# Kernel tuning notes

Hardware: AMD Instinct MI355X
Metric: run time of the kernel (lower is better)

## Reference

```python
import jax, jax.numpy as jnp
import numpy as np

B, L, D = 2, 2048, 1024
H, DK, DV = 16, 64, 64
LN_EPS = 1e-6


def setup_inputs() -> dict:
    key = jax.random.key(0)
    ks = jax.random.split(key, 8)
    s = 0.02
    return {
        "q": jax.random.normal(ks[0], (B, L, D), jnp.float32),
        "k": jax.random.normal(ks[1], (B, L, D), jnp.float32),
        "v": jax.random.normal(ks[2], (B, L, D), jnp.float32),
        "mask": jnp.ones((B, L, L), jnp.int32),
        "w_q": jax.random.normal(ks[3], (D, H * DK), jnp.float32) * s,
        "w_k": jax.random.normal(ks[4], (D, H * DK), jnp.float32) * s,
        "w_v": jax.random.normal(ks[5], (D, H * DV), jnp.float32) * s,
        "w_fc": jax.random.normal(ks[6], (H * DV, D), jnp.float32) * s,
        "ln_g": jnp.ones((D,), jnp.float32),
        "ln_b": jnp.zeros((D,), jnp.float32),
    }


def reference(q, k, v, mask, w_q, w_k, w_v, w_fc, ln_g, ln_b):
    b, lq, d = q.shape
    residual = q
    # QKV projections, split heads: (B, H, L, dk)
    qh = (q @ w_q).reshape(b, lq, H, DK).transpose(0, 2, 1, 3)
    kh = (k @ w_k).reshape(b, -1, H, DK).transpose(0, 2, 1, 3)
    vh = (v @ w_v).reshape(b, -1, H, DV).transpose(0, 2, 1, 3)
    scale = DK ** 0.5
    attn = jnp.einsum("bhqd,bhkd->bhqk", qh / scale, kh)
    attn = jnp.where(mask[:, None, :, :] == 0, -1e9, attn)
    attn = jax.nn.softmax(attn, axis=-1)  # dropout is identity in eval
    out = jnp.einsum("bhqk,bhkd->bhqd", attn, vh)
    out = out.transpose(0, 2, 1, 3).reshape(b, lq, H * DV)
    out = out @ w_fc + residual
    # LayerNorm (eps=1e-6)
    mu = out.mean(-1, keepdims=True)
    var = out.var(-1, keepdims=True)
    out = (out - mu) * jax.lax.rsqrt(var + LN_EPS) * ln_g + ln_b
    return out, attn
```

## Files before the change

kernel.cpp:

```cpp
#include <hip/hip_runtime.h>
#include <math.h>

static constexpr int Bc = 2;
static constexpr int Lc = 2048;
static constexpr int Dc = 1024;
static constexpr int Hc = 16;
static constexpr int DKc = 64;

typedef unsigned short u16;
typedef __attribute__((ext_vector_type(8))) short s16x8;
typedef __attribute__((ext_vector_type(4))) float f32x4;
typedef __attribute__((ext_vector_type(4))) unsigned short u16x4;

#define MFMA(a, b, c) __builtin_amdgcn_mfma_f32_16x16x32_bf16((a), (b), (c), 0, 0, 0)

__device__ __forceinline__ u16 f2bf(float f) {
    unsigned int u = __float_as_uint(f);
    u += 0x7fff + ((u >> 16) & 1);
    return (u16)(u >> 16);
}

__device__ __forceinline__ int swz(int row, int u) {
    return (row << 6) + ((u ^ (row & 7)) << 3);
}

__device__ __forceinline__ float blockReduce(float val, float* red) {
    __syncthreads();
    #pragma unroll
    for (int o = 32; o > 0; o >>= 1) val += __shfl_down(val, o, 64);
    const int lane = threadIdx.x & 63;
    const int wid = threadIdx.x >> 6;
    if (lane == 0) red[wid] = val;
    __syncthreads();
    if (threadIdx.x == 0) {
        float r = red[0];
        #pragma unroll
        for (int i = 1; i < 4; ++i) r += red[i];
        red[0] = r;
    }
    __syncthreads();
    return red[0];
}

__global__ __launch_bounds__(256) void k_wprep(const float* __restrict__ W,
                                               u16* __restrict__ Wt) {
    __shared__ float T[64][65];
    const int t = threadIdx.x;
    const int n0 = blockIdx.x * 64, k0 = blockIdx.y * 64;
    #pragma unroll
    for (int i = 0; i < 16; ++i) {
        int flat = t + i * 256;
        int r = flat >> 6, c = flat & 63;
        T[r][c] = W[(size_t)(k0 + r) * Dc + n0 + c];
    }
    __syncthreads();
    #pragma unroll
    for (int i = 0; i < 16; ++i) {
        int flat = t + i * 256;
        int r = flat >> 6, c = flat & 63;
        Wt[(size_t)(n0 + r) * Dc + k0 + c] = f2bf(T[c][r]);
    }
}

template<int MODE>
__global__ __launch_bounds__(256) void k_gemm(const void* __restrict__ Ap,
                                              const u16* __restrict__ Bt,
                                              const float* __restrict__ RES,
                                              void* __restrict__ Yp) {
    __shared__ u16 As[64 * 64];
    __shared__ u16 Bs[128 * 64];
    const int t = threadIdx.x;
    const int lane = t & 63, wid = t >> 6;
    const int wm = wid >> 1, wn = wid & 1;
    const int row0 = blockIdx.x * 64, col0 = blockIdx.y * 128;
    f32x4 acc[2][4] = {};
    for (int kt = 0; kt < Dc; kt += 64) {
        if constexpr (MODE == 0) {
            const float* A = (const float*)Ap;
            #pragma unroll
            for (int i = 0; i < 2; ++i) {
                int flat = t + i * 256;
                int r = flat >> 3, u = flat & 7;
                const float4* src = (const float4*)(A + (size_t)(row0 + r) * Dc + kt + u * 8);
                float4 x = src[0], y = src[1];
                union { s16x8 v; u16 q[8]; } pk;
                pk.q[0] = f2bf(x.x); pk.q[1] = f2bf(x.y); pk.q[2] = f2bf(x.z); pk.q[3] = f2bf(x.w);
                pk.q[4] = f2bf(y.x); pk.q[5] = f2bf(y.y); pk.q[6] = f2bf(y.z); pk.q[7] = f2bf(y.w);
                *(s16x8*)&As[swz(r, u)] = pk.v;
            }
        } else {
            const u16* A = (const u16*)Ap;
            #pragma unroll
            for (int i = 0; i < 2; ++i) {
                int flat = t + i * 256;
                int r = flat >> 3, u = flat & 7;
                *(s16x8*)&As[swz(r, u)] = *(const s16x8*)(A + (size_t)(row0 + r) * Dc + kt + u * 8);
            }
        }
        #pragma unroll
        for (int i = 0; i < 4; ++i) {
            int flat = t + i * 256;
            int r = flat >> 3, u = flat & 7;
            *(s16x8*)&Bs[swz(r, u)] = *(const s16x8*)(Bt + (size_t)(col0 + r) * Dc + kt + u * 8);
        }
        __syncthreads();
        #pragma unroll
        for (int ks = 0; ks < 2; ++ks) {
            const int u = ks * 4 + (lane >> 4);
            s16x8 a[2], b[4];
            #pragma unroll
            for (int m = 0; m < 2; ++m)
                a[m] = *(const s16x8*)&As[swz(wm * 32 + m * 16 + (lane & 15), u)];
            #pragma unroll
            for (int n = 0; n < 4; ++n)
                b[n] = *(const s16x8*)&Bs[swz(wn * 64 + n * 16 + (lane & 15), u)];
            #pragma unroll
            for (int m = 0; m < 2; ++m)
                #pragma unroll
                for (int n = 0; n < 4; ++n)
                    acc[m][n] = MFMA(a[m], b[n], acc[m][n]);
        }
        __syncthreads();
    }
    #pragma unroll
    for (int m = 0; m < 2; ++m) {
        #pragma unroll
        for (int i = 0; i < 4; ++i) {
            int r = row0 + wm * 32 + m * 16 + ((lane >> 4) << 2) + i;
            #pragma unroll
            for (int n = 0; n < 4; ++n) {
                int c = col0 + wn * 64 + n * 16 + (lane & 15);
                float val = acc[m][n][i];
                if constexpr (MODE == 0) {
                    u16* Y = (u16*)Yp;
                    int bb = r >> 11, l = r & (Lc - 1);
                    int h = c >> 6, dk = c & 63;
                    Y[(((size_t)(bb * Hc + h) * Lc) + l) * DKc + dk] = f2bf(val);
                } else {
                    float* Y = (float*)Yp;
                    Y[(size_t)r * Dc + c] = val + RES[(size_t)r * Dc + c];
                }
            }
        }
    }
}

__global__ __launch_bounds__(256) void k_scores(const u16* __restrict__ Qh,
                                                const u16* __restrict__ Kh,
                                                const int* __restrict__ mask,
                                                float* __restrict__ attn) {
    __shared__ u16 Qs[128 * 64];
    __shared__ u16 Ks[128 * 64];
    const int t = threadIdx.x;
    const int lane = t & 63, wid = t >> 6;
    const int wm = wid >> 1, wn = wid & 1;
    const int z = blockIdx.z, b = z >> 4;
    const int q0 = blockIdx.x * 128, c0 = blockIdx.y * 128;
    const u16* Qp = Qh + (size_t)z * Lc * DKc;
    const u16* Kp = Kh + (size_t)z * Lc * DKc;
    #pragma unroll
    for (int i = 0; i < 4; ++i) {
        int flat = t + i * 256;
        int r = flat >> 3, u = flat & 7;
        *(s16x8*)&Qs[swz(r, u)] = *(const s16x8*)(Qp + (size_t)(q0 + r) * DKc + u * 8);
        *(s16x8*)&Ks[swz(r, u)] = *(const s16x8*)(Kp + (size_t)(c0 + r) * DKc + u * 8);
    }
    __syncthreads();
    f32x4 acc[4][4] = {};
    #pragma unroll
    for (int ks = 0; ks < 2; ++ks) {
        const int u = ks * 4 + (lane >> 4);
        s16x8 a[4], bb[4];
        #pragma unroll
        for (int m = 0; m < 4; ++m)
            a[m] = *(const s16x8*)&Qs[swz(wm * 64 + m * 16 + (lane & 15), u)];
        #pragma unroll
        for (int n = 0; n < 4; ++n)
            bb[n] = *(const s16x8*)&Ks[swz(wn * 64 + n * 16 + (lane & 15), u)];
        #pragma unroll
        for (int m = 0; m < 4; ++m)
            #pragma unroll
            for (int n = 0; n < 4; ++n)
                acc[m][n] = MFMA(a[m], bb[n], acc[m][n]);
    }
    #pragma unroll
    for (int m = 0; m < 4; ++m) {
        #pragma unroll
        for (int i = 0; i < 4; ++i) {
            int q = q0 + wm * 64 + m * 16 + ((lane >> 4) << 2) + i;
            const int* mrow = mask + ((size_t)b * Lc + q) * Lc;
            float* arow = attn + ((size_t)z * Lc + q) * Lc;
            #pragma unroll
            for (int n = 0; n < 4; ++n) {
                int c = c0 + wn * 64 + n * 16 + (lane & 15);
                float s = acc[m][n][i] * 0.125f;
                if (mrow[c] == 0) s = -1e9f;
                arow[c] = s;
            }
        }
    }
}

__global__ __launch_bounds__(256) void k_softmax(float* __restrict__ attn) {
    const int lane = threadIdx.x & 63, wid = threadIdx.x >> 6;
    float4* p = (float4*)(attn + ((size_t)blockIdx.x * 4 + wid) * Lc);
    float4 v[8];
    float m = -INFINITY;
    #pragma unroll
    for (int j = 0; j < 8; ++j) {
        v[j] = p[lane + j * 64];
        m = fmaxf(m, fmaxf(fmaxf(v[j].x, v[j].y), fmaxf(v[j].z, v[j].w)));
    }
    #pragma unroll
    for (int o = 32; o > 0; o >>= 1) m = fmaxf(m, __shfl_xor(m, o, 64));
    float s = 0.f;
    #pragma unroll
    for (int j = 0; j < 8; ++j) {
        v[j].x = __expf(v[j].x - m); v[j].y = __expf(v[j].y - m);
        v[j].z = __expf(v[j].z - m); v[j].w = __expf(v[j].w - m);
        s += v[j].x + v[j].y + v[j].z + v[j].w;
    }
    #pragma unroll
    for (int o = 32; o > 0; o >>= 1) s += __shfl_xor(s, o, 64);
    const float inv = 1.0f / s;
    #pragma unroll
    for (int j = 0; j < 8; ++j) {
        v[j].x *= inv; v[j].y *= inv; v[j].z *= inv; v[j].w *= inv;
        p[lane + j * 64] = v[j];
    }
}

__global__ __launch_bounds__(256) void k_pv(const float* __restrict__ P,
                                            const u16* __restrict__ Vh,
                                            u16* __restrict__ AO) {
    __shared__ u16 Ps[64 * 64];
    __shared__ u16 Vt[64 * 64];
    const int t = threadIdx.x;
    const int lane = t & 63, wid = t >> 6;
    const int wm = wid >> 1, wn = wid & 1;
    const int z = blockIdx.z, b = z >> 4, h = z & 15;
    const int l0 = blockIdx.x * 64;
    const float* Pp = P + (size_t)z * Lc * Lc;
    const u16* Vp = Vh + (size_t)z * Lc * DKc;
    f32x4 acc[2][2] = {};
    for (int kt = 0; kt < Lc; kt += 64) {
        #pragma unroll
        for (int i = 0; i < 2; ++i) {
            int flat = t + i * 256;
            int r = flat >> 3, u = flat & 7;
            const float4* src = (const float4*)(Pp + (size_t)(l0 + r) * Lc + kt + u * 8);
            float4 x = src[0], y = src[1];
            union { s16x8 v; u16 q[8]; } pk;
            pk.q[0] = f2bf(x.x); pk.q[1] = f2bf(x.y); pk.q[2] = f2bf(x.z); pk.q[3] = f2bf(x.w);
            pk.q[4] = f2bf(y.x); pk.q[5] = f2bf(y.y); pk.q[6] = f2bf(y.z); pk.q[7] = f2bf(y.w);
            *(s16x8*)&Ps[swz(r, u)] = pk.v;
        }
        #pragma unroll
        for (int i = 0; i < 4; ++i) {
            int g = t + i * 256;
            int kv = g >> 4, dv0 = (g & 15) << 2;
            u16x4 vv = *(const u16x4*)(Vp + (size_t)(kt + kv) * DKc + dv0);
            int u2 = kv >> 3, klo = kv & 7;
            #pragma unroll
            for (int e = 0; e < 4; ++e) {
                int dv = dv0 + e;
                Vt[(dv << 6) + ((u2 ^ (dv & 7)) << 3) + klo] = vv[e];
            }
        }
        __syncthreads();
        #pragma unroll
        for (int ks = 0; ks < 2; ++ks) {
            const int u = ks * 4 + (lane >> 4);
            s16x8 a[2], bb[2];
            #pragma unroll
            for (int m = 0; m < 2; ++m)
                a[m] = *(const s16x8*)&Ps[swz(wm * 32 + m * 16 + (lane & 15), u)];
            #pragma unroll
            for (int n = 0; n < 2; ++n)
                bb[n] = *(const s16x8*)&Vt[swz(wn * 32 + n * 16 + (lane & 15), u)];
            #pragma unroll
            for (int m = 0; m < 2; ++m)
                #pragma unroll
                for (int n = 0; n < 2; ++n)
                    acc[m][n] = MFMA(a[m], bb[n], acc[m][n]);
        }
        __syncthreads();
    }
    #pragma unroll
    for (int m = 0; m < 2; ++m)
        #pragma unroll
        for (int i = 0; i < 4; ++i) {
            int l = l0 + wm * 32 + m * 16 + ((lane >> 4) << 2) + i;
            #pragma unroll
            for (int n = 0; n < 2; ++n) {
                int dv = wn * 32 + n * 16 + (lane & 15);
                AO[((size_t)(b * Lc + l)) * Dc + h * DKc + dv] = f2bf(acc[m][n][i]);
            }
        }
}

__global__ __launch_bounds__(256) void k_ln(const float* __restrict__ X,
                                            const float* __restrict__ g,
                                            const float* __restrict__ bta,
                                            float* __restrict__ Y) {
    __shared__ float red[8];
    const int row = blockIdx.x;
    const float4* x = (const float4*)(X + (size_t)row * Dc);
    const float4* g4 = (const float4*)g;
    const float4* b4 = (const float4*)bta;
    float4* y = (float4*)(Y + (size_t)row * Dc);
    const int tid = threadIdx.x;
    float4 v = x[tid];
    float s = v.x + v.y + v.z + v.w;
    float ss = v.x * v.x + v.y * v.y + v.z * v.z + v.w * v.w;
    s = blockReduce(s, red);
    ss = blockReduce(ss, red);
    const float mu = s * (1.0f / Dc);
    const float var = ss * (1.0f / Dc) - mu * mu;
    const float inv = rsqrtf(var + 1e-6f);
    float4 gv = g4[tid], bv = b4[tid], o;
    o.x = (v.x - mu) * inv * gv.x + bv.x;
    o.y = (v.y - mu) * inv * gv.y + bv.y;
    o.z = (v.z - mu) * inv * gv.z + bv.z;
    o.w = (v.w - mu) * inv * gv.w + bv.w;
    y[tid] = o;
}

extern "C" void kernel_launch(void* const* d_in, const int* in_sizes, int n_in,
                              void* d_out, int out_size, void* d_ws, size_t ws_size,
                              hipStream_t stream) {
    const float* q    = (const float*)d_in[0];
    const float* k    = (const float*)d_in[1];
    const float* v    = (const float*)d_in[2];
    const int*   mask = (const int*)d_in[3];
    const float* w_q  = (const float*)d_in[4];
    const float* w_k  = (const float*)d_in[5];
    const float* w_v  = (const float*)d_in[6];
    const float* w_fc = (const float*)d_in[7];
    const float* ln_g = (const float*)d_in[8];
    const float* ln_b = (const float*)d_in[9];

    float* out  = (float*)d_out;
    float* attn = out + (size_t)Bc * Lc * Dc;

    u16* ws = (u16*)d_ws;
    const size_t WSLOT = (size_t)Dc * Dc;
    const size_t HSLOT = (size_t)Bc * Hc * Lc * DKc;
    u16* wqT  = ws;
    u16* wkT  = wqT + WSLOT;
    u16* wvT  = wkT + WSLOT;
    u16* wfcT = wvT + WSLOT;
    u16* qh   = wfcT + WSLOT;
    u16* kh   = qh + HSLOT;
    u16* vh   = kh + HSLOT;
    u16* ao   = vh + HSLOT;

    dim3 blk(256);
    k_wprep<<<dim3(16, 16), blk, 0, stream>>>(w_q, wqT);
    k_wprep<<<dim3(16, 16), blk, 0, stream>>>(w_k, wkT);
    k_wprep<<<dim3(16, 16), blk, 0, stream>>>(w_v, wvT);
    k_wprep<<<dim3(16, 16), blk, 0, stream>>>(w_fc, wfcT);

    k_gemm<0><<<dim3(64, 8), blk, 0, stream>>>(q, wqT, nullptr, qh);
    k_gemm<0><<<dim3(64, 8), blk, 0, stream>>>(k, wkT, nullptr, kh);
    k_gemm<0><<<dim3(64, 8), blk, 0, stream>>>(v, wvT, nullptr, vh);

    k_scores<<<dim3(16, 16, 32), blk, 0, stream>>>(qh, kh, mask, attn);
    k_softmax<<<dim3(16384), blk, 0, stream>>>(attn);
    k_pv<<<dim3(32, 1, 32), blk, 0, stream>>>(attn, vh, ao);

    k_gemm<1><<<dim3(64, 8), blk, 0, stream>>>(ao, wfcT, q, out);
    k_ln<<<dim3(Bc * Lc), blk, 0, stream>>>(out, ln_g, ln_b, out);
}
```

Baseline: 1.200 ms.

## Fuse scores, softmax and PV into a two-pass attention kernel with a bit-packed mask

Replaces the separate scores, softmax and PV kernels with one kernel per (q-tile, head). The first pass computes QK^T and keeps running row max and sum. The second pass recomputes the scores, writes normalized probabilities to attn once, and feeds them from LDS in bf16 to the PV MFMA. The mask is packed into bitwords by a ballot kernel, and V is pre-transposed in a separate kernel. Together these remove the write and read-back round trips of the large fp32 attn matrix and the int32 mask reads, at the cost of computing QK^T twice and having fewer blocks in flight.

```diff
diff --git a/kernel.cpp b/kernel.cpp
--- a/kernel.cpp
+++ b/kernel.cpp
@@ -10,7 +10,6 @@
 typedef unsigned short u16;
 typedef __attribute__((ext_vector_type(8))) short s16x8;
 typedef __attribute__((ext_vector_type(4))) float f32x4;
-typedef __attribute__((ext_vector_type(4))) unsigned short u16x4;
 
 #define MFMA(a, b, c) __builtin_amdgcn_mfma_f32_16x16x32_bf16((a), (b), (c), 0, 0, 0)
 
@@ -22,6 +21,9 @@
 
 __device__ __forceinline__ int swz(int row, int u) {
     return (row << 6) + ((u ^ (row & 7)) << 3);
+}
+__device__ __forceinline__ int swz128(int row, int u) {
+    return (row << 7) + ((u ^ (row & 7)) << 3);
 }
 
 __device__ __forceinline__ float blockReduce(float val, float* red) {
@@ -42,6 +44,15 @@
     return red[0];
 }
 
+__global__ __launch_bounds__(256) void k_mpack(const int* __restrict__ mask,
+                                               unsigned* __restrict__ pm) {
+    size_t gid = (size_t)blockIdx.x * 256 + threadIdx.x;
+    int v = mask[gid];
+    unsigned long long b = __ballot(v != 0);
+    int lane = threadIdx.x & 63;
+    if ((lane & 31) == 0) pm[gid >> 5] = (unsigned)(b >> (lane & 32));
+}
+
 __global__ __launch_bounds__(256) void k_wprep(const float* __restrict__ W,
                                                u16* __restrict__ Wt) {
     __shared__ float T[64][65];
@@ -59,6 +70,36 @@
         int flat = t + i * 256;
         int r = flat >> 6, c = flat & 63;
         Wt[(size_t)(n0 + r) * Dc + k0 + c] = f2bf(T[c][r]);
+    }
+}
+
+__global__ __launch_bounds__(256) void k_vtrans(const u16* __restrict__ Vh,
+                                                u16* __restrict__ Vt) {
+    __shared__ u16 T[64 * 72];
+    const int t = threadIdx.x;
+    const int z = blockIdx.y;
+    const int c0 = blockIdx.x * 64;
+    const u16* src = Vh + (size_t)z * Lc * DKc;
+    #pragma unroll
+    for (int i = 0; i < 2; ++i) {
+        int flat = t + i * 256;
+        int r = flat >> 3, u = flat & 7;
+        *(s16x8*)&T[r * 72 + ((u ^ ((r >> 3) & 7)) << 3)] =
+            *(const s16x8*)(src + (size_t)(c0 + r) * DKc + u * 8);
+    }
+    __syncthreads();
+    u16* dst = Vt + (size_t)z * DKc * Lc;
+    #pragma unroll
+    for (int i = 0; i < 2; ++i) {
+        int flat = t + i * 256;
+        int dv = flat >> 3, uc = flat & 7;
+        union { s16x8 v; u16 q[8]; } o;
+        #pragma unroll
+        for (int e = 0; e < 8; ++e) {
+            int cc = uc * 8 + e;
+            o.q[e] = T[cc * 72 + (((dv >> 3) ^ ((cc >> 3) & 7)) << 3) + (dv & 7)];
+        }
+        *(s16x8*)(dst + (size_t)dv * Lc + c0 + uc * 8) = o.v;
     }
 }
 
@@ -145,157 +186,153 @@
     }
 }
 
-__global__ __launch_bounds__(256) void k_scores(const u16* __restrict__ Qh,
-                                                const u16* __restrict__ Kh,
-                                                const int* __restrict__ mask,
-                                                float* __restrict__ attn) {
-    __shared__ u16 Qs[128 * 64];
+__global__ __launch_bounds__(256) void k_attn(const u16* __restrict__ Qh,
+                                              const u16* __restrict__ Kh,
+                                              const u16* __restrict__ Vt,
+                                              const unsigned* __restrict__ pm,
+                                              float* __restrict__ attn,
+                                              u16* __restrict__ AO) {
+    __shared__ u16 Qs[64 * 64];
     __shared__ u16 Ks[128 * 64];
+    __shared__ u16 Vs[64 * 128];
+    __shared__ u16 Ps[64 * 128];
     const int t = threadIdx.x;
-    const int lane = t & 63, wid = t >> 6;
-    const int wm = wid >> 1, wn = wid & 1;
-    const int z = blockIdx.z, b = z >> 4;
-    const int q0 = blockIdx.x * 128, c0 = blockIdx.y * 128;
+    const int lane = t & 63, w = t >> 6;
+    const int z = blockIdx.y, b = z >> 4, h = z & 15;
+    const int q0 = blockIdx.x * 64;
     const u16* Qp = Qh + (size_t)z * Lc * DKc;
     const u16* Kp = Kh + (size_t)z * Lc * DKc;
-    #pragma unroll
-    for (int i = 0; i < 4; ++i) {
+    const u16* Vp = Vt + (size_t)z * DKc * Lc;
+
+    #pragma unroll
+    for (int i = 0; i < 2; ++i) {
         int flat = t + i * 256;
         int r = flat >> 3, u = flat & 7;
         *(s16x8*)&Qs[swz(r, u)] = *(const s16x8*)(Qp + (size_t)(q0 + r) * DKc + u * 8);
-        *(s16x8*)&Ks[swz(r, u)] = *(const s16x8*)(Kp + (size_t)(c0 + r) * DKc + u * 8);
-    }
-    __syncthreads();
-    f32x4 acc[4][4] = {};
-    #pragma unroll
-    for (int ks = 0; ks < 2; ++ks) {
-        const int u = ks * 4 + (lane >> 4);
-        s16x8 a[4], bb[4];
-        #pragma unroll
-        for (int m = 0; m < 4; ++m)
-            a[m] = *(const s16x8*)&Qs[swz(wm * 64 + m * 16 + (lane & 15), u)];
-        #pragma unroll
-        for (int n = 0; n < 4; ++n)
-            bb[n] = *(const s16x8*)&Ks[swz(wn * 64 + n * 16 + (lane & 15), u)];
-        #pragma unroll
-        for (int m = 0; m < 4; ++m)
-            #pragma unroll
-            for (int n = 0; n < 4; ++n)
-                acc[m][n] = MFMA(a[m], bb[n], acc[m][n]);
-    }
-    #pragma unroll
-    for (int m = 0; m < 4; ++m) {
-        #pragma unroll
-        for (int i = 0; i < 4; ++i) {
-            int q = q0 + wm * 64 + m * 16 + ((lane >> 4) << 2) + i;
-            const int* mrow = mask + ((size_t)b * Lc + q) * Lc;
-            float* arow = attn + ((size_t)z * Lc + q) * Lc;
-            #pragma unroll
-            for (int n = 0; n < 4; ++n) {
-                int c = c0 + wn * 64 + n * 16 + (lane & 15);
-                float s = acc[m][n][i] * 0.125f;
-                if (mrow[c] == 0) s = -1e9f;
-                arow[c] = s;
-            }
-        }
-    }
-}
-
-__global__ __launch_bounds__(256) void k_softmax(float* __restrict__ attn) {
-    const int lane = threadIdx.x & 63, wid = threadIdx.x >> 6;
-    float4* p = (float4*)(attn + ((size_t)blockIdx.x * 4 + wid) * Lc);
-    float4 v[8];
-    float m = -INFINITY;
-    #pragma unroll
-    for (int j = 0; j < 8; ++j) {
-        v[j] = p[lane + j * 64];
-        m = fmaxf(m, fmaxf(fmaxf(v[j].x, v[j].y), fmaxf(v[j].z, v[j].w)));
-    }
-    #pragma unroll
-    for (int o = 32; o > 0; o >>= 1) m = fmaxf(m, __shfl_xor(m, o, 64));
-    float s = 0.f;
-    #pragma unroll
-    for (int j = 0; j < 8; ++j) {
-        v[j].x = __expf(v[j].x - m); v[j].y = __expf(v[j].y - m);
-        v[j].z = __expf(v[j].z - m); v[j].w = __expf(v[j].w - m);
-        s += v[j].x + v[j].y + v[j].z + v[j].w;
-    }
-    #pragma unroll
-    for (int o = 32; o > 0; o >>= 1) s += __shfl_xor(s, o, 64);
-    const float inv = 1.0f / s;
-    #pragma unroll
-    for (int j = 0; j < 8; ++j) {
-        v[j].x *= inv; v[j].y *= inv; v[j].z *= inv; v[j].w *= inv;
-        p[lane + j * 64] = v[j];
-    }
-}
-
-__global__ __launch_bounds__(256) void k_pv(const float* __restrict__ P,
-                                            const u16* __restrict__ Vh,
-                                            u16* __restrict__ AO) {
-    __shared__ u16 Ps[64 * 64];
-    __shared__ u16 Vt[64 * 64];
-    const int t = threadIdx.x;
-    const int lane = t & 63, wid = t >> 6;
-    const int wm = wid >> 1, wn = wid & 1;
-    const int z = blockIdx.z, b = z >> 4, h = z & 15;
-    const int l0 = blockIdx.x * 64;
-    const float* Pp = P + (size_t)z * Lc * Lc;
-    const u16* Vp = Vh + (size_t)z * Lc * DKc;
-    f32x4 acc[2][2] = {};
-    for (int kt = 0; kt < Lc; kt += 64) {
-        #pragma unroll
-        for (int i = 0; i < 2; ++i) {
+    }
+    const int rq = w * 16 + ((lane >> 4) << 2);
+    float mrow[4], lrow[4];
+    #pragma unroll
+    for (int i = 0; i < 4; ++i) { mrow[i] = -1e9f; lrow[i] = 0.f; }
+
+    for (int ct = 0; ct < 16; ++ct) {
+        __syncthreads();
+        #pragma unroll
+        for (int i = 0; i < 4; ++i) {
             int flat = t + i * 256;
             int r = flat >> 3, u = flat & 7;
-            const float4* src = (const float4*)(Pp + (size_t)(l0 + r) * Lc + kt + u * 8);
-            float4 x = src[0], y = src[1];
-            union { s16x8 v; u16 q[8]; } pk;
-            pk.q[0] = f2bf(x.x); pk.q[1] = f2bf(x.y); pk.q[2] = f2bf(x.z); pk.q[3] = f2bf(x.w);
-            pk.q[4] = f2bf(y.x); pk.q[5] = f2bf(y.y); pk.q[6] = f2bf(y.z); pk.q[7] = f2bf(y.w);
-            *(s16x8*)&Ps[swz(r, u)] = pk.v;
-        }
-        #pragma unroll
-        for (int i = 0; i < 4; ++i) {
-            int g = t + i * 256;
-            int kv = g >> 4, dv0 = (g & 15) << 2;
-            u16x4 vv = *(const u16x4*)(Vp + (size_t)(kt + kv) * DKc + dv0);
-            int u2 = kv >> 3, klo = kv & 7;
-            #pragma unroll
-            for (int e = 0; e < 4; ++e) {
-                int dv = dv0 + e;
-                Vt[(dv << 6) + ((u2 ^ (dv & 7)) << 3) + klo] = vv[e];
-            }
-        }
-        __syncthreads();
+            *(s16x8*)&Ks[swz(r, u)] = *(const s16x8*)(Kp + (size_t)(ct * 128 + r) * DKc + u * 8);
+        }
+        __syncthreads();
+        f32x4 sf[8] = {};
         #pragma unroll
         for (int ks = 0; ks < 2; ++ks) {
             const int u = ks * 4 + (lane >> 4);
-            s16x8 a[2], bb[2];
-            #pragma unroll
-            for (int m = 0; m < 2; ++m)
-                a[m] = *(const s16x8*)&Ps[swz(wm * 32 + m * 16 + (lane & 15), u)];
-            #pragma unroll
-            for (int n = 0; n < 2; ++n)
-                bb[n] = *(const s16x8*)&Vt[swz(wn * 32 + n * 16 + (lane & 15), u)];
-            #pragma unroll
-            for (int m = 0; m < 2; ++m)
-                #pragma unroll
-                for (int n = 0; n < 2; ++n)
-                    acc[m][n] = MFMA(a[m], bb[n], acc[m][n]);
-        }
-        __syncthreads();
-    }
-    #pragma unroll
-    for (int m = 0; m < 2; ++m)
-        #pragma unroll
-        for (int i = 0; i < 4; ++i) {
-            int l = l0 + wm * 32 + m * 16 + ((lane >> 4) << 2) + i;
-            #pragma unroll
-            for (int n = 0; n < 2; ++n) {
-                int dv = wn * 32 + n * 16 + (lane & 15);
-                AO[((size_t)(b * Lc + l)) * Dc + h * DKc + dv] = f2bf(acc[m][n][i]);
-            }
+            s16x8 a = *(const s16x8*)&Qs[swz(w * 16 + (lane & 15), u)];
+            #pragma unroll
+            for (int n = 0; n < 8; ++n) {
+                s16x8 bb = *(const s16x8*)&Ks[swz(n * 16 + (lane & 15), u)];
+                sf[n] = MFMA(a, bb, sf[n]);
+            }
+        }
+        #pragma unroll
+        for (int i = 0; i < 4; ++i) {
+            int q = q0 + rq + i;
+            const unsigned* pmr = pm + (((size_t)b * Lc + q) << 6) + ct * 4;
+            unsigned mw0 = pmr[0], mw1 = pmr[1], mw2 = pmr[2], mw3 = pmr[3];
+            float vals[8];
+            float rmax = -1e9f;
+            #pragma unroll
+            for (int n = 0; n < 8; ++n) {
+                unsigned mw = (n < 2) ? mw0 : (n < 4) ? mw1 : (n < 6) ? mw2 : mw3;
+                unsigned bit = (mw >> ((n & 1) * 16 + (lane & 15))) & 1u;
+                float s = sf[n][i] * 0.125f;
+                s = bit ? s : -1e9f;
+                vals[n] = s;
+                rmax = fmaxf(rmax, s);
+            }
+            #pragma unroll
+            for (int o = 1; o < 16; o <<= 1) rmax = fmaxf(rmax, __shfl_xor(rmax, o, 64));
+            float mnew = fmaxf(mrow[i], rmax);
+            float corr = __expf(mrow[i] - mnew);
+            float ssum = 0.f;
+            #pragma unroll
+            for (int n = 0; n < 8; ++n) ssum += __expf(vals[n] - mnew);
+            #pragma unroll
+            for (int o = 1; o < 16; o <<= 1) ssum += __shfl_xor(ssum, o, 64);
+            lrow[i] = lrow[i] * corr + ssum;
+            mrow[i] = mnew;
+        }
+    }
+    float invl[4];
+    #pragma unroll
+    for (int i = 0; i < 4; ++i) invl[i] = 1.0f / lrow[i];
+
+    f32x4 oacc[4] = {};
+    for (int ct = 0; ct < 16; ++ct) {
+        __syncthreads();
+        #pragma unroll
+        for (int i = 0; i < 4; ++i) {
+            int flat = t + i * 256;
+            int r = flat >> 3, u = flat & 7;
+            *(s16x8*)&Ks[swz(r, u)] = *(const s16x8*)(Kp + (size_t)(ct * 128 + r) * DKc + u * 8);
+        }
+        #pragma unroll
+        for (int i = 0; i < 4; ++i) {
+            int flat = t + i * 256;
+            int dv = flat >> 4, u = flat & 15;
+            *(s16x8*)&Vs[swz128(dv, u)] = *(const s16x8*)(Vp + (size_t)dv * Lc + ct * 128 + u * 8);
+        }
+        __syncthreads();
+        f32x4 sf[8] = {};
+        #pragma unroll
+        for (int ks = 0; ks < 2; ++ks) {
+            const int u = ks * 4 + (lane >> 4);
+            s16x8 a = *(const s16x8*)&Qs[swz(w * 16 + (lane & 15), u)];
+            #pragma unroll
+            for (int n = 0; n < 8; ++n) {
+                s16x8 bb = *(const s16x8*)&Ks[swz(n * 16 + (lane & 15), u)];
+                sf[n] = MFMA(a, bb, sf[n]);
+            }
+        }
+        #pragma unroll
+        for (int i = 0; i < 4; ++i) {
+            int q = q0 + rq + i;
+            int r = rq + i;
+            const unsigned* pmr = pm + (((size_t)b * Lc + q) << 6) + ct * 4;
+            unsigned mw0 = pmr[0], mw1 = pmr[1], mw2 = pmr[2], mw3 = pmr[3];
+            float* arow = attn + ((size_t)z * Lc + q) * Lc + ct * 128;
+            #pragma unroll
+            for (int n = 0; n < 8; ++n) {
+                unsigned mw = (n < 2) ? mw0 : (n < 4) ? mw1 : (n < 6) ? mw2 : mw3;
+                unsigned bit = (mw >> ((n & 1) * 16 + (lane & 15))) & 1u;
+                float s = sf[n][i] * 0.125f;
+                s = bit ? s : -1e9f;
+                float p = __expf(s - mrow[i]) * invl[i];
+                int c = n * 16 + (lane & 15);
+                arow[c] = p;
+                Ps[(r << 7) + ((((c >> 3) ^ (r & 7)) << 3)) + (c & 7)] = f2bf(p);
+            }
+        }
+        #pragma unroll
+        for (int ks = 0; ks < 4; ++ks) {
+            const int u = ks * 4 + (lane >> 4);
+            const int ar = w * 16 + (lane & 15);
+            s16x8 a = *(const s16x8*)&Ps[swz128(ar, u)];
+            #pragma unroll
+            for (int n = 0; n < 4; ++n) {
+                int dv = n * 16 + (lane & 15);
+                s16x8 bb = *(const s16x8*)&Vs[swz128(dv, u)];
+                oacc[n] = MFMA(a, bb, oacc[n]);
+            }
+        }
+    }
+    #pragma unroll
+    for (int n = 0; n < 4; ++n)
+        #pragma unroll
+        for (int i = 0; i < 4; ++i) {
+            int q = q0 + rq + i;
+            AO[((size_t)(b * Lc + q)) * Dc + h * DKc + n * 16 + (lane & 15)] = f2bf(oacc[n][i]);
         }
 }
 
@@ -351,23 +388,25 @@
     u16* wvT  = wkT + WSLOT;
     u16* wfcT = wvT + WSLOT;
     u16* qh   = wfcT + WSLOT;
-    u16* kh   = qh + HSLOT;
+    u16* vt   = qh + HSLOT;
+    u16* kh   = vt + HSLOT;
     u16* vh   = kh + HSLOT;
-    u16* ao   = vh + HSLOT;
+    u16* ao   = vh;
+    unsigned* pm = (unsigned*)(vh + HSLOT);
 
     dim3 blk(256);
+    k_mpack<<<dim3((Bc * Lc * Lc) / 256), blk, 0, stream>>>(mask, pm);
     k_wprep<<<dim3(16, 16), blk, 0, stream>>>(w_q, wqT);
     k_wprep<<<dim3(16, 16), blk, 0, stream>>>(w_k, wkT);
     k_wprep<<<dim3(16, 16), blk, 0, stream>>>(w_v, wvT);
     k_wprep<<<dim3(16, 16), blk, 0, stream>>>(w_fc, wfcT);
 
+    k_gemm<0><<<dim3(64, 8), blk, 0, stream>>>(v, wvT, nullptr, vh);
+    k_vtrans<<<dim3(32, 32), blk, 0, stream>>>(vh, vt);
     k_gemm<0><<<dim3(64, 8), blk, 0, stream>>>(q, wqT, nullptr, qh);
     k_gemm<0><<<dim3(64, 8), blk, 0, stream>>>(k, wkT, nullptr, kh);
-    k_gemm<0><<<dim3(64, 8), blk, 0, stream>>>(v, wvT, nullptr, vh);
-
-    k_scores<<<dim3(16, 16, 32), blk, 0, stream>>>(qh, kh, mask, attn);
-    k_softmax<<<dim3(16384), blk, 0, stream>>>(attn);
-    k_pv<<<dim3(32, 1, 32), blk, 0, stream>>>(attn, vh, ao);
+
+    k_attn<<<dim3(32, 32), blk, 0, stream>>>(qh, kh, vt, pm, attn, ao);
 
     k_gemm<1><<<dim3(64, 8), blk, 0, stream>>>(ao, wfcT, q, out);
     k_ln<<<dim3(Bc * Lc), blk, 0, stream>>>(out, ln_g, ln_b, out);
```

New measurement: 1.030 ms. 14.2% less time.
